# Performance work log

Measured on AMD Instinct MI355X. Metric: run time of the kernel, lower is better.

Reference implementation:

```python
import jax, jax.numpy as jnp
import numpy as np

B, N, D = 4, 4096, 256


def setup_inputs() -> dict:
    key = jax.random.key(0)
    ks = jax.random.split(key, 8)
    s = 0.05
    return {
        "x": jax.random.normal(ks[0], (B, N, D), dtype=jnp.float32),
        "z": jax.random.normal(ks[1], (B, N, D), dtype=jnp.float32),
        "Wq_w": jax.random.normal(ks[2], (D, D), dtype=jnp.float32) * s,
        "Wq_b": jax.random.normal(ks[3], (D,), dtype=jnp.float32) * s,
        "Wk_w": jax.random.normal(ks[4], (D, D), dtype=jnp.float32) * s,
        "Wk_b": jax.random.normal(ks[5], (D,), dtype=jnp.float32) * s,
        "Wv_w": jax.random.normal(ks[6], (D, D), dtype=jnp.float32) * s,
        "Wv_b": jax.random.normal(ks[7], (D,), dtype=jnp.float32) * s,
    }


def reference(x, z, Wq_w, Wq_b, Wk_w, Wk_b, Wv_w, Wv_b):
    # torch Linear: y = x @ W.T + b
    q = jnp.einsum("bnd,ed->bne", x, Wq_w) + Wq_b  # [B,N,D]
    k = jnp.einsum("bnd,ed->bne", z, Wk_w) + Wk_b  # [B,N,D]
    v = jnp.einsum("bnd,ed->bne", z, Wv_w) + Wv_b  # [B,N,D]
    inv_sqrt_d = 1.0 / jnp.sqrt(jnp.float32(q.shape[-1]))
    s = jnp.einsum("bqd,bkd->bqk", q, k) * inv_sqrt_d  # [B,N,N] scores
    attn = jax.nn.softmax(s, axis=-1)
    return jnp.einsum("bqk,bkd->bqd", attn, v)
```

## Files before the change

kernel.cpp:

```cpp
#include <hip/hip_runtime.h>
#include <hip/hip_bf16.h>
#include <math.h>

#define BATCH 4
#define SEQ   4096
#define DIM   256
#define AS1 __attribute__((address_space(1)))
#define AS3 __attribute__((address_space(3)))

typedef __attribute__((ext_vector_type(8))) short  bf16x8;
typedef __attribute__((ext_vector_type(4))) short  bf16x4;
typedef __attribute__((ext_vector_type(4))) float  f32x4;
typedef __attribute__((ext_vector_type(4))) int    i32x4;

#define LOG2E 1.44269504088896340736f
#define EXP2(x) __builtin_amdgcn_exp2f(x)

__device__ __forceinline__ short f2bf(float f) {
    union { float f; unsigned u; } v; v.f = f;
    unsigned r = (v.u + 0x7fffu + ((v.u >> 16) & 1u)) >> 16;
    return (short)r;
}

__device__ __forceinline__ int cvtpk(float lo, float hi) {
    int r;
    asm("v_cvt_pk_bf16_f32 %0, %1, %2" : "=v"(r) : "v"(lo), "v"(hi));
    return r;
}

__device__ __forceinline__ void gload_lds16(const void* g, void* l) {
    __builtin_amdgcn_global_load_lds((const AS1 void*)g, (AS3 void*)l, 16, 0, 0);
}

template<bool TRANS>
__global__ __launch_bounds__(512) void proj_kernel(
    const float* __restrict__ A,
    const float* __restrict__ W,
    const float* __restrict__ bias,
    unsigned short* __restrict__ out,
    float scale)
{
    __shared__ __align__(16) short Wlds[256 * 40];

    const int t    = threadIdx.x;
    const int wave = t >> 6, lane = t & 63;
    const int rw   = wave & 3, nh = wave >> 2;
    const int c    = lane & 15, g = lane >> 4;
    const int wrow = blockIdx.x * 64 + rw * 16;

    f32x4 acc[8];
    for (int nt = 0; nt < 8; ++nt) acc[nt] = f32x4{0.f, 0.f, 0.f, 0.f};

    f32x4 wpf[4];
    for (int i = 0; i < 4; ++i) {
        int f = i * 2048 + t * 4;
        wpf[i] = *(const f32x4*)&W[(f >> 5) * 256 + (f & 31)];
    }
    f32x4 a0 = *(const f32x4*)&A[(wrow + c) * 256 + g * 8];
    f32x4 a1 = *(const f32x4*)&A[(wrow + c) * 256 + g * 8 + 4];

    for (int ks = 0; ks < 8; ++ks) {
        __syncthreads();
        for (int i = 0; i < 4; ++i) {
            int f = i * 2048 + t * 4;
            bf16x4 s4;
            s4[0] = f2bf(wpf[i][0]); s4[1] = f2bf(wpf[i][1]);
            s4[2] = f2bf(wpf[i][2]); s4[3] = f2bf(wpf[i][3]);
            *(bf16x4*)&Wlds[(f >> 5) * 40 + (f & 31)] = s4;
        }
        __syncthreads();
        bf16x8 af;
        af[0] = f2bf(a0[0]); af[1] = f2bf(a0[1]); af[2] = f2bf(a0[2]); af[3] = f2bf(a0[3]);
        af[4] = f2bf(a1[0]); af[5] = f2bf(a1[1]); af[6] = f2bf(a1[2]); af[7] = f2bf(a1[3]);
        if (ks < 7) {
            for (int i = 0; i < 4; ++i) {
                int f = i * 2048 + t * 4;
                wpf[i] = *(const f32x4*)&W[(f >> 5) * 256 + (ks + 1) * 32 + (f & 31)];
            }
            a0 = *(const f32x4*)&A[(wrow + c) * 256 + (ks + 1) * 32 + g * 8];
            a1 = *(const f32x4*)&A[(wrow + c) * 256 + (ks + 1) * 32 + g * 8 + 4];
        }
        __builtin_amdgcn_s_setprio(1);
        for (int nt = 0; nt < 8; ++nt) {
            int e = (nh * 8 + nt) * 16 + c;
            bf16x8 bfr = *(const bf16x8*)&Wlds[e * 40 + g * 8];
            acc[nt] = __builtin_amdgcn_mfma_f32_16x16x32_bf16(af, bfr, acc[nt], 0, 0, 0);
        }
        __builtin_amdgcn_s_setprio(0);
    }

    if constexpr (TRANS) {
        const int nb = wrow >> 12, n0 = wrow & 4095;
        for (int nt = 0; nt < 8; ++nt) {
            int e = (nh * 8 + nt) * 16 + c;
            float bv = bias[e];
            bf16x4 s4;
            s4[0] = f2bf((acc[nt][0] + bv) * scale); s4[1] = f2bf((acc[nt][1] + bv) * scale);
            s4[2] = f2bf((acc[nt][2] + bv) * scale); s4[3] = f2bf((acc[nt][3] + bv) * scale);
            *(bf16x4*)&out[((size_t)nb * DIM + e) * SEQ + n0 + g * 4] = s4;
        }
    } else {
        for (int nt = 0; nt < 8; ++nt) {
            int e = (nh * 8 + nt) * 16 + c;
            float bv = bias[e];
            for (int j = 0; j < 4; ++j)
                out[(size_t)(wrow + g * 4 + j) * 256 + e] =
                    (unsigned short)f2bf((acc[nt][j] + bv) * scale);
        }
    }
}

__global__ __launch_bounds__(512) void kv_proj_kernel(
    const float* __restrict__ A,
    const float* __restrict__ Wk, const float* __restrict__ bk,
    const float* __restrict__ Wv, const float* __restrict__ bv,
    unsigned short* __restrict__ Kout,
    unsigned short* __restrict__ Vtout)
{
    __shared__ __align__(16) short WldsK[256 * 40];
    __shared__ __align__(16) short WldsV[256 * 40];

    const int t    = threadIdx.x;
    const int wave = t >> 6, lane = t & 63;
    const int rw   = wave & 3, nh = wave >> 2;
    const int c    = lane & 15, g = lane >> 4;
    const int wrow = blockIdx.x * 64 + rw * 16;

    f32x4 acck[8], accv[8];
    for (int nt = 0; nt < 8; ++nt) {
        acck[nt] = f32x4{0.f, 0.f, 0.f, 0.f};
        accv[nt] = f32x4{0.f, 0.f, 0.f, 0.f};
    }

    f32x4 wpfk[4], wpfv[4];
    for (int i = 0; i < 4; ++i) {
        int f = i * 2048 + t * 4;
        wpfk[i] = *(const f32x4*)&Wk[(f >> 5) * 256 + (f & 31)];
        wpfv[i] = *(const f32x4*)&Wv[(f >> 5) * 256 + (f & 31)];
    }
    f32x4 a0 = *(const f32x4*)&A[(wrow + c) * 256 + g * 8];
    f32x4 a1 = *(const f32x4*)&A[(wrow + c) * 256 + g * 8 + 4];

    for (int ks = 0; ks < 8; ++ks) {
        __syncthreads();
        for (int i = 0; i < 4; ++i) {
            int f = i * 2048 + t * 4;
            bf16x4 sk, sv;
            sk[0] = f2bf(wpfk[i][0]); sk[1] = f2bf(wpfk[i][1]);
            sk[2] = f2bf(wpfk[i][2]); sk[3] = f2bf(wpfk[i][3]);
            sv[0] = f2bf(wpfv[i][0]); sv[1] = f2bf(wpfv[i][1]);
            sv[2] = f2bf(wpfv[i][2]); sv[3] = f2bf(wpfv[i][3]);
            *(bf16x4*)&WldsK[(f >> 5) * 40 + (f & 31)] = sk;
            *(bf16x4*)&WldsV[(f >> 5) * 40 + (f & 31)] = sv;
        }
        __syncthreads();
        bf16x8 af;
        af[0] = f2bf(a0[0]); af[1] = f2bf(a0[1]); af[2] = f2bf(a0[2]); af[3] = f2bf(a0[3]);
        af[4] = f2bf(a1[0]); af[5] = f2bf(a1[1]); af[6] = f2bf(a1[2]); af[7] = f2bf(a1[3]);
        if (ks < 7) {
            for (int i = 0; i < 4; ++i) {
                int f = i * 2048 + t * 4;
                wpfk[i] = *(const f32x4*)&Wk[(f >> 5) * 256 + (ks + 1) * 32 + (f & 31)];
                wpfv[i] = *(const f32x4*)&Wv[(f >> 5) * 256 + (ks + 1) * 32 + (f & 31)];
            }
            a0 = *(const f32x4*)&A[(wrow + c) * 256 + (ks + 1) * 32 + g * 8];
            a1 = *(const f32x4*)&A[(wrow + c) * 256 + (ks + 1) * 32 + g * 8 + 4];
        }
        __builtin_amdgcn_s_setprio(1);
        for (int nt = 0; nt < 8; ++nt) {
            int e = (nh * 8 + nt) * 16 + c;
            bf16x8 bk_ = *(const bf16x8*)&WldsK[e * 40 + g * 8];
            acck[nt] = __builtin_amdgcn_mfma_f32_16x16x32_bf16(af, bk_, acck[nt], 0, 0, 0);
            bf16x8 bv_ = *(const bf16x8*)&WldsV[e * 40 + g * 8];
            accv[nt] = __builtin_amdgcn_mfma_f32_16x16x32_bf16(af, bv_, accv[nt], 0, 0, 0);
        }
        __builtin_amdgcn_s_setprio(0);
    }

    for (int nt = 0; nt < 8; ++nt) {
        int e = (nh * 8 + nt) * 16 + c;
        float bb = bk[e];
        for (int j = 0; j < 4; ++j)
            Kout[(size_t)(wrow + g * 4 + j) * 256 + e] =
                (unsigned short)f2bf(acck[nt][j] + bb);
    }
    const int nb = wrow >> 12, n0 = wrow & 4095;
    for (int nt = 0; nt < 8; ++nt) {
        int e = (nh * 8 + nt) * 16 + c;
        float bb = bv[e];
        bf16x4 s4;
        s4[0] = f2bf(accv[nt][0] + bb); s4[1] = f2bf(accv[nt][1] + bb);
        s4[2] = f2bf(accv[nt][2] + bb); s4[3] = f2bf(accv[nt][3] + bb);
        *(bf16x4*)&Vtout[((size_t)nb * DIM + e) * SEQ + n0 + g * 4] = s4;
    }
}

#define KVB 32

__global__ __launch_bounds__(256, 2) void fa2_kernel(
    const unsigned short* __restrict__ Q,
    const unsigned short* __restrict__ K,
    const unsigned short* __restrict__ Vt,
    unsigned short* __restrict__ Opart,
    float2* __restrict__ ml,
    int nsplit)
{
    __shared__ __align__(16) unsigned short Klds[2][KVB * 256];
    __shared__ __align__(16) unsigned short Vlds[2][256 * KVB];

    const int t = threadIdx.x;
    const int w = t >> 6, lane = t & 63;
    const int c = lane & 15, g = lane >> 4;

    int b, sidx, qt;
    if (nsplit == 4) {
        int xcd  = blockIdx.x & 7;
        int rest = blockIdx.x >> 3;
        int combo = (xcd << 1) | (rest >> 5);
        qt   = rest & 31;
        b    = combo >> 2;
        sidx = combo & 3;
    } else {
        qt   = blockIdx.x & 31;
        b    = blockIdx.x >> 5;
        sidx = 0;
    }
    const int ts = (sidx * 128) / nsplit;
    const int te = ((sidx + 1) * 128) / nsplit;

    const int wrow = qt * 128 + w * 32;

    bf16x8 qf[2][8];
    #pragma unroll
    for (int h = 0; h < 2; ++h) {
        const unsigned short* Qrow = &Q[((size_t)b * SEQ + wrow + 16 * h + c) * DIM];
        #pragma unroll
        for (int ks = 0; ks < 8; ++ks)
            qf[h][ks] = *(const bf16x8*)&Qrow[ks * 32 + g * 8];
    }

    f32x4 o[2][16];
    #pragma unroll
    for (int h = 0; h < 2; ++h)
        #pragma unroll
        for (int nt = 0; nt < 16; ++nt) o[h][nt] = f32x4{0.f, 0.f, 0.f, 0.f};
    float m[2]     = {-1e30f, -1e30f};
    float llane[2] = {0.f, 0.f};

    const char* Kb_ = (const char*)&K[(size_t)b * SEQ * DIM];
    const char* Vb_ = (const char*)&Vt[(size_t)b * DIM * SEQ];

    const int l31 = lane & 31;
    int koff[4], voff[4], dstb[4];
    const int vsw = ((lane >> 2) & 3) ^ ((lane >> 4) & 3);
    const int vcb = ((lane & 3) ^ vsw) << 4;
    #pragma unroll
    for (int ii = 0; ii < 4; ++ii) {
        int kr = 8 * w + 2 * ii + (lane >> 5);
        int sc = (kr & 3) | ((kr & 8) >> 1);
        koff[ii] = kr * 512 + ((l31 ^ sc) << 4);
        int vr = 64 * w + 16 * ii + (lane >> 2);
        voff[ii] = vr * (SEQ * 2) + vcb;
        dstb[ii] = (4 * w + ii) * 1024;
    }

    #define STAGE(kt_, buf_) do {                                              \
        const size_t kb_ = (size_t)(kt_) * (KVB * DIM * 2);                    \
        const size_t vb_ = (size_t)(kt_) * (KVB * 2);                          \
        _Pragma("unroll")                                                      \
        for (int ii = 0; ii < 4; ++ii) {                                       \
            gload_lds16(Kb_ + kb_ + koff[ii], (char*)&Klds[buf_][0] + dstb[ii]); \
            gload_lds16(Vb_ + vb_ + voff[ii], (char*)&Vlds[buf_][0] + dstb[ii]); \
        }                                                                      \
    } while (0)

    STAGE(ts, 0);
    int buf = 0;

    const int xk   = (c & 7) << 3;
    const int rphi = ((c & 3) + 8 * (c >> 2));
    const int vcol = (g * 8) ^ ((((c & 3) ^ ((c >> 2) & 3))) << 3);

    for (int kt = ts; kt < te; ++kt) {
        asm volatile("s_waitcnt vmcnt(0)" ::: "memory");
        __builtin_amdgcn_s_barrier();
        if (kt + 1 < te) STAGE(kt + 1, buf ^ 1);

        const unsigned short* Kl = &Klds[buf][0];
        const unsigned short* Vl = &Vlds[buf][0];

        f32x4 s[2][2];
        #pragma unroll
        for (int h = 0; h < 2; ++h) {
            s[h][0] = f32x4{0.f, 0.f, 0.f, 0.f};
            s[h][1] = f32x4{0.f, 0.f, 0.f, 0.f};
        }
        __builtin_amdgcn_s_setprio(1);
        #pragma unroll
        for (int ks = 0; ks < 8; ++ks) {
            int off = (ks * 32 + g * 8) ^ xk;
            bf16x8 kf0 = *(const bf16x8*)&Kl[rphi * 256 + off];
            bf16x8 kf1 = *(const bf16x8*)&Kl[(rphi + 4) * 256 + off];
            s[0][0] = __builtin_amdgcn_mfma_f32_16x16x32_bf16(kf0, qf[0][ks], s[0][0], 0, 0, 0);
            s[1][0] = __builtin_amdgcn_mfma_f32_16x16x32_bf16(kf0, qf[1][ks], s[1][0], 0, 0, 0);
            s[0][1] = __builtin_amdgcn_mfma_f32_16x16x32_bf16(kf1, qf[0][ks], s[0][1], 0, 0, 0);
            s[1][1] = __builtin_amdgcn_mfma_f32_16x16x32_bf16(kf1, qf[1][ks], s[1][1], 0, 0, 0);
        }
        __builtin_amdgcn_s_setprio(0);

        float pm[2];
        #pragma unroll
        for (int h = 0; h < 2; ++h)
            pm[h] = fmaxf(fmaxf(fmaxf(s[h][0][0], s[h][0][1]), fmaxf(s[h][0][2], s[h][0][3])),
                          fmaxf(fmaxf(s[h][1][0], s[h][1][1]), fmaxf(s[h][1][2], s[h][1][3])));
        bool ok = (pm[0] <= m[0] + 11.f) && (pm[1] <= m[1] + 11.f);
        if (!__all(ok)) {
            #pragma unroll
            for (int h = 0; h < 2; ++h) {
                float pr = pm[h];
                pr = fmaxf(pr, __shfl_xor(pr, 16));
                pr = fmaxf(pr, __shfl_xor(pr, 32));
                float mn = fmaxf(m[h], pr);
                float r  = EXP2(m[h] - mn);
                m[h] = mn; llane[h] *= r;
                float r0 = __shfl(r, g * 4 + 0), r1 = __shfl(r, g * 4 + 1);
                float r2 = __shfl(r, g * 4 + 2), r3 = __shfl(r, g * 4 + 3);
                #pragma unroll
                for (int nt = 0; nt < 16; ++nt) {
                    o[0][nt][0] *= (h == 0 ? r0 : 1.f);
                }
                if (h == 0) {
                    #pragma unroll
                    for (int nt = 0; nt < 16; ++nt) {
                        o[0][nt][0] *= r0; o[0][nt][1] *= r1;
                        o[0][nt][2] *= r2; o[0][nt][3] *= r3;
                    }
                } else {
                    #pragma unroll
                    for (int nt = 0; nt < 16; ++nt) {
                        o[1][nt][0] *= r0; o[1][nt][1] *= r1;
                        o[1][nt][2] *= r2; o[1][nt][3] *= r3;
                    }
                }
            }
        }
        bf16x8 pa0, pa1;
        {
            float p0 = EXP2(s[0][0][0] - m[0]), p1 = EXP2(s[0][0][1] - m[0]);
            float p2 = EXP2(s[0][0][2] - m[0]), p3 = EXP2(s[0][0][3] - m[0]);
            float p4 = EXP2(s[0][1][0] - m[0]), p5 = EXP2(s[0][1][1] - m[0]);
            float p6 = EXP2(s[0][1][2] - m[0]), p7 = EXP2(s[0][1][3] - m[0]);
            llane[0] += ((p0 + p1) + (p2 + p3)) + ((p4 + p5) + (p6 + p7));
            union { int d[4]; bf16x8 v; } u;
            u.d[0] = cvtpk(p0, p1); u.d[1] = cvtpk(p2, p3);
            u.d[2] = cvtpk(p4, p5); u.d[3] = cvtpk(p6, p7);
            pa0 = u.v;
        }
        {
            float p0 = EXP2(s[1][0][0] - m[1]), p1 = EXP2(s[1][0][1] - m[1]);
            float p2 = EXP2(s[1][0][2] - m[1]), p3 = EXP2(s[1][0][3] - m[1]);
            float p4 = EXP2(s[1][1][0] - m[1]), p5 = EXP2(s[1][1][1] - m[1]);
            float p6 = EXP2(s[1][1][2] - m[1]), p7 = EXP2(s[1][1][3] - m[1]);
            llane[1] += ((p0 + p1) + (p2 + p3)) + ((p4 + p5) + (p6 + p7));
            union { int d[4]; bf16x8 v; } u;
            u.d[0] = cvtpk(p0, p1); u.d[1] = cvtpk(p2, p3);
            u.d[2] = cvtpk(p4, p5); u.d[3] = cvtpk(p6, p7);
            pa1 = u.v;
        }

        __builtin_amdgcn_s_setprio(1);
        #pragma unroll
        for (int nt = 0; nt < 16; ++nt) {
            bf16x8 vf = *(const bf16x8*)&Vl[(nt * 16 + c) * 32 + vcol];
            o[0][nt] = __builtin_amdgcn_mfma_f32_16x16x32_bf16(pa0, vf, o[0][nt], 0, 0, 0);
            o[1][nt] = __builtin_amdgcn_mfma_f32_16x16x32_bf16(pa1, vf, o[1][nt], 0, 0, 0);
        }
        __builtin_amdgcn_s_setprio(0);
        buf ^= 1;
    }

    #pragma unroll
    for (int h = 0; h < 2; ++h) {
        float lsum = llane[h];
        lsum += __shfl_xor(lsum, 16);
        lsum += __shfl_xor(lsum, 32);
        float inv = 1.0f / lsum;
        float i0 = __shfl(inv, g * 4 + 0), i1 = __shfl(inv, g * 4 + 1);
        float i2 = __shfl(inv, g * 4 + 2), i3 = __shfl(inv, g * 4 + 3);

        const size_t obase = ((size_t)sidx * BATCH * SEQ + (size_t)b * SEQ + wrow + 16 * h) * DIM;
        for (int nt = 0; nt < 16; ++nt) {
            Opart[obase + (size_t)(g * 4 + 0) * DIM + nt * 16 + c] =
                (unsigned short)f2bf(o[h][nt][0] * i0);
            Opart[obase + (size_t)(g * 4 + 1) * DIM + nt * 16 + c] =
                (unsigned short)f2bf(o[h][nt][1] * i1);
            Opart[obase + (size_t)(g * 4 + 2) * DIM + nt * 16 + c] =
                (unsigned short)f2bf(o[h][nt][2] * i2);
            Opart[obase + (size_t)(g * 4 + 3) * DIM + nt * 16 + c] =
                (unsigned short)f2bf(o[h][nt][3] * i3);
        }
        if (g == 0) {
            ml[(size_t)sidx * BATCH * SEQ + (size_t)b * SEQ + wrow + 16 * h + c] =
                make_float2(m[h], lsum);
        }
    }
}

__global__ __launch_bounds__(256) void combine_kernel(
    const unsigned short* __restrict__ Opart, const float2* __restrict__ ml,
    float* __restrict__ out)
{
    const int t = threadIdx.x;
    const size_t row = (size_t)blockIdx.x * 4 + (t >> 6);
    const int lane = t & 63;

    float2 e[4];
    float M = -1e30f;
    for (int s = 0; s < 4; ++s) {
        e[s] = ml[(size_t)s * BATCH * SEQ + row];
        M = fmaxf(M, e[s].x);
    }
    float wgt[4], L = 0.f;
    for (int s = 0; s < 4; ++s) { wgt[s] = e[s].y * EXP2(e[s].x - M); L += wgt[s]; }
    float invL = 1.0f / L;

    f32x4 acc = f32x4{0.f, 0.f, 0.f, 0.f};
    for (int s = 0; s < 4; ++s) {
        bf16x4 v = *(const bf16x4*)&Opart[((size_t)s * BATCH * SEQ + row) * DIM + lane * 4];
        float ws = wgt[s] * invL;
        union { unsigned u; float f; } c0, c1, c2, c3;
        c0.u = ((unsigned)(unsigned short)v[0]) << 16;
        c1.u = ((unsigned)(unsigned short)v[1]) << 16;
        c2.u = ((unsigned)(unsigned short)v[2]) << 16;
        c3.u = ((unsigned)(unsigned short)v[3]) << 16;
        acc[0] += ws * c0.f; acc[1] += ws * c1.f;
        acc[2] += ws * c2.f; acc[3] += ws * c3.f;
    }
    *(f32x4*)&out[row * DIM + lane * 4] = acc;
}

__global__ void expand_kernel(const unsigned short* __restrict__ in,
                              float* __restrict__ o) {
    size_t i = (size_t)blockIdx.x * blockDim.x + threadIdx.x;
    union { unsigned u; float f; } v;
    v.u = ((unsigned)in[i]) << 16;
    o[i] = v.f;
}

extern "C" void kernel_launch(void* const* d_in, const int* in_sizes, int n_in,
                              void* d_out, int out_size, void* d_ws, size_t ws_size,
                              hipStream_t stream) {
    const float* x  = (const float*)d_in[0];
    const float* z  = (const float*)d_in[1];
    const float* Wq = (const float*)d_in[2];
    const float* bq = (const float*)d_in[3];
    const float* Wk = (const float*)d_in[4];
    const float* bk = (const float*)d_in[5];
    const float* Wv = (const float*)d_in[6];
    const float* bv = (const float*)d_in[7];
    float* out = (float*)d_out;

    const size_t TENS = (size_t)BATCH * SEQ * DIM;
    unsigned short* Qb  = (unsigned short*)d_ws;
    unsigned short* Kb  = Qb + TENS;
    unsigned short* Vtb = Kb + TENS;

    const size_t base_bytes = 3 * TENS * sizeof(unsigned short);
    const size_t need4 = base_bytes + 4 * TENS * sizeof(unsigned short)
                       + 4 * (size_t)BATCH * SEQ * sizeof(float2);
    const int nsplit = (ws_size >= need4) ? 4 : 1;

    const float qscale = 0.0625f * LOG2E;

    proj_kernel<false><<<256, 512, 0, stream>>>(x, Wq, bq, Qb, qscale);
    kv_proj_kernel<<<256, 512, 0, stream>>>(z, Wk, bk, Wv, bv, Kb, Vtb);

    if (nsplit == 4) {
        unsigned short* Op = (unsigned short*)((char*)d_ws + base_bytes);
        float2* mlb = (float2*)((char*)d_ws + base_bytes + 4 * TENS * sizeof(unsigned short));
        fa2_kernel<<<512, 256, 0, stream>>>(Qb, Kb, Vtb, Op, mlb, 4);
        combine_kernel<<<4096, 256, 0, stream>>>(Op, mlb, out);
    } else {
        unsigned short* Op = (unsigned short*)((char*)d_ws + base_bytes);
        float2* mlb = (float2*)((char*)d_ws + base_bytes + TENS * sizeof(unsigned short));
        fa2_kernel<<<128, 256, 0, stream>>>(Qb, Kb, Vtb, Op, mlb, 1);
        expand_kernel<<<TENS / 256, 256, 0, stream>>>(Op, out);
    }
}
```

Before: 122.9 us.

## Merge Q and KV projections into one launch, widen combine loads

Folds the Q projection and the fused K/V projection into a single 512-block launch, with the first 256 blocks computing Q and the rest computing K and V. This removes one kernel launch and lets both projections share the GPU at once. It also deletes a redundant per-tile rescale loop in the attention kernel that multiplied o[0] by r0, a multiply the following h==0 block appears to perform as well. The combine kernel now has each lane handle 8 bf16 values with 16-byte loads and launches half as many blocks. The merged kernel always allocates LDS for two weight tiles, which may reduce occupancy for the Q blocks.

```diff
diff --git a/kernel.cpp b/kernel.cpp
--- a/kernel.cpp
+++ b/kernel.cpp
@@ -32,166 +32,146 @@
     __builtin_amdgcn_global_load_lds((const AS1 void*)g, (AS3 void*)l, 16, 0, 0);
 }
 
-template<bool TRANS>
-__global__ __launch_bounds__(512) void proj_kernel(
-    const float* __restrict__ A,
-    const float* __restrict__ W,
-    const float* __restrict__ bias,
-    unsigned short* __restrict__ out,
-    float scale)
+__global__ __launch_bounds__(512) void qkv_proj_kernel(
+    const float* __restrict__ x, const float* __restrict__ z,
+    const float* __restrict__ Wq, const float* __restrict__ bq,
+    const float* __restrict__ Wk, const float* __restrict__ bk,
+    const float* __restrict__ Wv, const float* __restrict__ bv,
+    unsigned short* __restrict__ Qout,
+    unsigned short* __restrict__ Kout,
+    unsigned short* __restrict__ Vtout,
+    float qscale)
 {
-    __shared__ __align__(16) short Wlds[256 * 40];
+    __shared__ __align__(16) short WldsA[256 * 40];
+    __shared__ __align__(16) short WldsB[256 * 40];
 
     const int t    = threadIdx.x;
     const int wave = t >> 6, lane = t & 63;
     const int rw   = wave & 3, nh = wave >> 2;
     const int c    = lane & 15, g = lane >> 4;
-    const int wrow = blockIdx.x * 64 + rw * 16;
-
-    f32x4 acc[8];
-    for (int nt = 0; nt < 8; ++nt) acc[nt] = f32x4{0.f, 0.f, 0.f, 0.f};
-
-    f32x4 wpf[4];
-    for (int i = 0; i < 4; ++i) {
-        int f = i * 2048 + t * 4;
-        wpf[i] = *(const f32x4*)&W[(f >> 5) * 256 + (f & 31)];
-    }
-    f32x4 a0 = *(const f32x4*)&A[(wrow + c) * 256 + g * 8];
-    f32x4 a1 = *(const f32x4*)&A[(wrow + c) * 256 + g * 8 + 4];
-
-    for (int ks = 0; ks < 8; ++ks) {
-        __syncthreads();
+
+    if (blockIdx.x < 256) {
+        const int wrow = blockIdx.x * 64 + rw * 16;
+        f32x4 acc[8];
+        #pragma unroll
+        for (int nt = 0; nt < 8; ++nt) acc[nt] = f32x4{0.f, 0.f, 0.f, 0.f};
+
+        f32x4 wpf[4];
         for (int i = 0; i < 4; ++i) {
             int f = i * 2048 + t * 4;
-            bf16x4 s4;
-            s4[0] = f2bf(wpf[i][0]); s4[1] = f2bf(wpf[i][1]);
-            s4[2] = f2bf(wpf[i][2]); s4[3] = f2bf(wpf[i][3]);
-            *(bf16x4*)&Wlds[(f >> 5) * 40 + (f & 31)] = s4;
-        }
-        __syncthreads();
-        bf16x8 af;
-        af[0] = f2bf(a0[0]); af[1] = f2bf(a0[1]); af[2] = f2bf(a0[2]); af[3] = f2bf(a0[3]);
-        af[4] = f2bf(a1[0]); af[5] = f2bf(a1[1]); af[6] = f2bf(a1[2]); af[7] = f2bf(a1[3]);
-        if (ks < 7) {
+            wpf[i] = *(const f32x4*)&Wq[(f >> 5) * 256 + (f & 31)];
+        }
+        f32x4 a0 = *(const f32x4*)&x[(wrow + c) * 256 + g * 8];
+        f32x4 a1 = *(const f32x4*)&x[(wrow + c) * 256 + g * 8 + 4];
+
+        for (int ks = 0; ks < 8; ++ks) {
+            __syncthreads();
             for (int i = 0; i < 4; ++i) {
                 int f = i * 2048 + t * 4;
-                wpf[i] = *(const f32x4*)&W[(f >> 5) * 256 + (ks + 1) * 32 + (f & 31)];
-            }
-            a0 = *(const f32x4*)&A[(wrow + c) * 256 + (ks + 1) * 32 + g * 8];
-            a1 = *(const f32x4*)&A[(wrow + c) * 256 + (ks + 1) * 32 + g * 8 + 4];
-        }
-        __builtin_amdgcn_s_setprio(1);
+                bf16x4 s4;
+                s4[0] = f2bf(wpf[i][0]); s4[1] = f2bf(wpf[i][1]);
+                s4[2] = f2bf(wpf[i][2]); s4[3] = f2bf(wpf[i][3]);
+                *(bf16x4*)&WldsA[(f >> 5) * 40 + (f & 31)] = s4;
+            }
+            __syncthreads();
+            bf16x8 af;
+            af[0] = f2bf(a0[0]); af[1] = f2bf(a0[1]); af[2] = f2bf(a0[2]); af[3] = f2bf(a0[3]);
+            af[4] = f2bf(a1[0]); af[5] = f2bf(a1[1]); af[6] = f2bf(a1[2]); af[7] = f2bf(a1[3]);
+            if (ks < 7) {
+                for (int i = 0; i < 4; ++i) {
+                    int f = i * 2048 + t * 4;
+                    wpf[i] = *(const f32x4*)&Wq[(f >> 5) * 256 + (ks + 1) * 32 + (f & 31)];
+                }
+                a0 = *(const f32x4*)&x[(wrow + c) * 256 + (ks + 1) * 32 + g * 8];
+                a1 = *(const f32x4*)&x[(wrow + c) * 256 + (ks + 1) * 32 + g * 8 + 4];
+            }
+            __builtin_amdgcn_s_setprio(1);
+            #pragma unroll
+            for (int nt = 0; nt < 8; ++nt) {
+                int e = (nh * 8 + nt) * 16 + c;
+                bf16x8 bfr = *(const bf16x8*)&WldsA[e * 40 + g * 8];
+                acc[nt] = __builtin_amdgcn_mfma_f32_16x16x32_bf16(af, bfr, acc[nt], 0, 0, 0);
+            }
+            __builtin_amdgcn_s_setprio(0);
+        }
         for (int nt = 0; nt < 8; ++nt) {
             int e = (nh * 8 + nt) * 16 + c;
-            bf16x8 bfr = *(const bf16x8*)&Wlds[e * 40 + g * 8];
-            acc[nt] = __builtin_amdgcn_mfma_f32_16x16x32_bf16(af, bfr, acc[nt], 0, 0, 0);
-        }
-        __builtin_amdgcn_s_setprio(0);
-    }
-
-    if constexpr (TRANS) {
+            float bv_ = bq[e];
+            for (int j = 0; j < 4; ++j)
+                Qout[(size_t)(wrow + g * 4 + j) * 256 + e] =
+                    (unsigned short)f2bf((acc[nt][j] + bv_) * qscale);
+        }
+    } else {
+        const int wrow = (blockIdx.x - 256) * 64 + rw * 16;
+        f32x4 acck[8], accv[8];
+        #pragma unroll
+        for (int nt = 0; nt < 8; ++nt) {
+            acck[nt] = f32x4{0.f, 0.f, 0.f, 0.f};
+            accv[nt] = f32x4{0.f, 0.f, 0.f, 0.f};
+        }
+
+        f32x4 wpfk[4], wpfv[4];
+        for (int i = 0; i < 4; ++i) {
+            int f = i * 2048 + t * 4;
+            wpfk[i] = *(const f32x4*)&Wk[(f >> 5) * 256 + (f & 31)];
+            wpfv[i] = *(const f32x4*)&Wv[(f >> 5) * 256 + (f & 31)];
+        }
+        f32x4 a0 = *(const f32x4*)&z[(wrow + c) * 256 + g * 8];
+        f32x4 a1 = *(const f32x4*)&z[(wrow + c) * 256 + g * 8 + 4];
+
+        for (int ks = 0; ks < 8; ++ks) {
+            __syncthreads();
+            for (int i = 0; i < 4; ++i) {
+                int f = i * 2048 + t * 4;
+                bf16x4 sk, sv;
+                sk[0] = f2bf(wpfk[i][0]); sk[1] = f2bf(wpfk[i][1]);
+                sk[2] = f2bf(wpfk[i][2]); sk[3] = f2bf(wpfk[i][3]);
+                sv[0] = f2bf(wpfv[i][0]); sv[1] = f2bf(wpfv[i][1]);
+                sv[2] = f2bf(wpfv[i][2]); sv[3] = f2bf(wpfv[i][3]);
+                *(bf16x4*)&WldsA[(f >> 5) * 40 + (f & 31)] = sk;
+                *(bf16x4*)&WldsB[(f >> 5) * 40 + (f & 31)] = sv;
+            }
+            __syncthreads();
+            bf16x8 af;
+            af[0] = f2bf(a0[0]); af[1] = f2bf(a0[1]); af[2] = f2bf(a0[2]); af[3] = f2bf(a0[3]);
+            af[4] = f2bf(a1[0]); af[5] = f2bf(a1[1]); af[6] = f2bf(a1[2]); af[7] = f2bf(a1[3]);
+            if (ks < 7) {
+                for (int i = 0; i < 4; ++i) {
+                    int f = i * 2048 + t * 4;
+                    wpfk[i] = *(const f32x4*)&Wk[(f >> 5) * 256 + (ks + 1) * 32 + (f & 31)];
+                    wpfv[i] = *(const f32x4*)&Wv[(f >> 5) * 256 + (ks + 1) * 32 + (f & 31)];
+                }
+                a0 = *(const f32x4*)&z[(wrow + c) * 256 + (ks + 1) * 32 + g * 8];
+                a1 = *(const f32x4*)&z[(wrow + c) * 256 + (ks + 1) * 32 + g * 8 + 4];
+            }
+            __builtin_amdgcn_s_setprio(1);
+            #pragma unroll
+            for (int nt = 0; nt < 8; ++nt) {
+                int e = (nh * 8 + nt) * 16 + c;
+                bf16x8 bk_ = *(const bf16x8*)&WldsA[e * 40 + g * 8];
+                acck[nt] = __builtin_amdgcn_mfma_f32_16x16x32_bf16(af, bk_, acck[nt], 0, 0, 0);
+                bf16x8 bv_ = *(const bf16x8*)&WldsB[e * 40 + g * 8];
+                accv[nt] = __builtin_amdgcn_mfma_f32_16x16x32_bf16(af, bv_, accv[nt], 0, 0, 0);
+            }
+            __builtin_amdgcn_s_setprio(0);
+        }
+
+        for (int nt = 0; nt < 8; ++nt) {
+            int e = (nh * 8 + nt) * 16 + c;
+            float bb = bk[e];
+            for (int j = 0; j < 4; ++j)
+                Kout[(size_t)(wrow + g * 4 + j) * 256 + e] =
+                    (unsigned short)f2bf(acck[nt][j] + bb);
+        }
         const int nb = wrow >> 12, n0 = wrow & 4095;
         for (int nt = 0; nt < 8; ++nt) {
             int e = (nh * 8 + nt) * 16 + c;
-            float bv = bias[e];
+            float bb = bv[e];
             bf16x4 s4;
-            s4[0] = f2bf((acc[nt][0] + bv) * scale); s4[1] = f2bf((acc[nt][1] + bv) * scale);
-            s4[2] = f2bf((acc[nt][2] + bv) * scale); s4[3] = f2bf((acc[nt][3] + bv) * scale);
-            *(bf16x4*)&out[((size_t)nb * DIM + e) * SEQ + n0 + g * 4] = s4;
-        }
-    } else {
-        for (int nt = 0; nt < 8; ++nt) {
-            int e = (nh * 8 + nt) * 16 + c;
-            float bv = bias[e];
-            for (int j = 0; j < 4; ++j)
-                out[(size_t)(wrow + g * 4 + j) * 256 + e] =
-                    (unsigned short)f2bf((acc[nt][j] + bv) * scale);
-        }
-    }
-}
-
-__global__ __launch_bounds__(512) void kv_proj_kernel(
-    const float* __restrict__ A,
-    const float* __restrict__ Wk, const float* __restrict__ bk,
-    const float* __restrict__ Wv, const float* __restrict__ bv,
-    unsigned short* __restrict__ Kout,
-    unsigned short* __restrict__ Vtout)
-{
-    __shared__ __align__(16) short WldsK[256 * 40];
-    __shared__ __align__(16) short WldsV[256 * 40];
-
-    const int t    = threadIdx.x;
-    const int wave = t >> 6, lane = t & 63;
-    const int rw   = wave & 3, nh = wave >> 2;
-    const int c    = lane & 15, g = lane >> 4;
-    const int wrow = blockIdx.x * 64 + rw * 16;
-
-    f32x4 acck[8], accv[8];
-    for (int nt = 0; nt < 8; ++nt) {
-        acck[nt] = f32x4{0.f, 0.f, 0.f, 0.f};
-        accv[nt] = f32x4{0.f, 0.f, 0.f, 0.f};
-    }
-
-    f32x4 wpfk[4], wpfv[4];
-    for (int i = 0; i < 4; ++i) {
-        int f = i * 2048 + t * 4;
-        wpfk[i] = *(const f32x4*)&Wk[(f >> 5) * 256 + (f & 31)];
-        wpfv[i] = *(const f32x4*)&Wv[(f >> 5) * 256 + (f & 31)];
-    }
-    f32x4 a0 = *(const f32x4*)&A[(wrow + c) * 256 + g * 8];
-    f32x4 a1 = *(const f32x4*)&A[(wrow + c) * 256 + g * 8 + 4];
-
-    for (int ks = 0; ks < 8; ++ks) {
-        __syncthreads();
-        for (int i = 0; i < 4; ++i) {
-            int f = i * 2048 + t * 4;
-            bf16x4 sk, sv;
-            sk[0] = f2bf(wpfk[i][0]); sk[1] = f2bf(wpfk[i][1]);
-            sk[2] = f2bf(wpfk[i][2]); sk[3] = f2bf(wpfk[i][3]);
-            sv[0] = f2bf(wpfv[i][0]); sv[1] = f2bf(wpfv[i][1]);
-            sv[2] = f2bf(wpfv[i][2]); sv[3] = f2bf(wpfv[i][3]);
-            *(bf16x4*)&WldsK[(f >> 5) * 40 + (f & 31)] = sk;
-            *(bf16x4*)&WldsV[(f >> 5) * 40 + (f & 31)] = sv;
-        }
-        __syncthreads();
-        bf16x8 af;
-        af[0] = f2bf(a0[0]); af[1] = f2bf(a0[1]); af[2] = f2bf(a0[2]); af[3] = f2bf(a0[3]);
-        af[4] = f2bf(a1[0]); af[5] = f2bf(a1[1]); af[6] = f2bf(a1[2]); af[7] = f2bf(a1[3]);
-        if (ks < 7) {
-            for (int i = 0; i < 4; ++i) {
-                int f = i * 2048 + t * 4;
-                wpfk[i] = *(const f32x4*)&Wk[(f >> 5) * 256 + (ks + 1) * 32 + (f & 31)];
-                wpfv[i] = *(const f32x4*)&Wv[(f >> 5) * 256 + (ks + 1) * 32 + (f & 31)];
-            }
-            a0 = *(const f32x4*)&A[(wrow + c) * 256 + (ks + 1) * 32 + g * 8];
-            a1 = *(const f32x4*)&A[(wrow + c) * 256 + (ks + 1) * 32 + g * 8 + 4];
-        }
-        __builtin_amdgcn_s_setprio(1);
-        for (int nt = 0; nt < 8; ++nt) {
-            int e = (nh * 8 + nt) * 16 + c;
-            bf16x8 bk_ = *(const bf16x8*)&WldsK[e * 40 + g * 8];
-            acck[nt] = __builtin_amdgcn_mfma_f32_16x16x32_bf16(af, bk_, acck[nt], 0, 0, 0);
-            bf16x8 bv_ = *(const bf16x8*)&WldsV[e * 40 + g * 8];
-            accv[nt] = __builtin_amdgcn_mfma_f32_16x16x32_bf16(af, bv_, accv[nt], 0, 0, 0);
-        }
-        __builtin_amdgcn_s_setprio(0);
-    }
-
-    for (int nt = 0; nt < 8; ++nt) {
-        int e = (nh * 8 + nt) * 16 + c;
-        float bb = bk[e];
-        for (int j = 0; j < 4; ++j)
-            Kout[(size_t)(wrow + g * 4 + j) * 256 + e] =
-                (unsigned short)f2bf(acck[nt][j] + bb);
-    }
-    const int nb = wrow >> 12, n0 = wrow & 4095;
-    for (int nt = 0; nt < 8; ++nt) {
-        int e = (nh * 8 + nt) * 16 + c;
-        float bb = bv[e];
-        bf16x4 s4;
-        s4[0] = f2bf(accv[nt][0] + bb); s4[1] = f2bf(accv[nt][1] + bb);
-        s4[2] = f2bf(accv[nt][2] + bb); s4[3] = f2bf(accv[nt][3] + bb);
-        *(bf16x4*)&Vtout[((size_t)nb * DIM + e) * SEQ + n0 + g * 4] = s4;
+            s4[0] = f2bf(accv[nt][0] + bb); s4[1] = f2bf(accv[nt][1] + bb);
+            s4[2] = f2bf(accv[nt][2] + bb); s4[3] = f2bf(accv[nt][3] + bb);
+            *(bf16x4*)&Vtout[((size_t)nb * DIM + e) * SEQ + n0 + g * 4] = s4;
+        }
     }
 }
 
@@ -325,10 +305,6 @@
                 m[h] = mn; llane[h] *= r;
                 float r0 = __shfl(r, g * 4 + 0), r1 = __shfl(r, g * 4 + 1);
                 float r2 = __shfl(r, g * 4 + 2), r3 = __shfl(r, g * 4 + 3);
-                #pragma unroll
-                for (int nt = 0; nt < 16; ++nt) {
-                    o[0][nt][0] *= (h == 0 ? r0 : 1.f);
-                }
                 if (h == 0) {
                     #pragma unroll
                     for (int nt = 0; nt < 16; ++nt) {
@@ -411,32 +387,38 @@
     float* __restrict__ out)
 {
     const int t = threadIdx.x;
-    const size_t row = (size_t)blockIdx.x * 4 + (t >> 6);
-    const int lane = t & 63;
+    const size_t row = (size_t)blockIdx.x * 8 + (t >> 5);
+    const int lane = t & 31;
 
     float2 e[4];
     float M = -1e30f;
+    #pragma unroll
     for (int s = 0; s < 4; ++s) {
         e[s] = ml[(size_t)s * BATCH * SEQ + row];
         M = fmaxf(M, e[s].x);
     }
     float wgt[4], L = 0.f;
+    #pragma unroll
     for (int s = 0; s < 4; ++s) { wgt[s] = e[s].y * EXP2(e[s].x - M); L += wgt[s]; }
     float invL = 1.0f / L;
 
-    f32x4 acc = f32x4{0.f, 0.f, 0.f, 0.f};
+    float acc[8] = {0.f, 0.f, 0.f, 0.f, 0.f, 0.f, 0.f, 0.f};
+    #pragma unroll
     for (int s = 0; s < 4; ++s) {
-        bf16x4 v = *(const bf16x4*)&Opart[((size_t)s * BATCH * SEQ + row) * DIM + lane * 4];
+        bf16x8 v = *(const bf16x8*)&Opart[((size_t)s * BATCH * SEQ + row) * DIM + lane * 8];
         float ws = wgt[s] * invL;
-        union { unsigned u; float f; } c0, c1, c2, c3;
-        c0.u = ((unsigned)(unsigned short)v[0]) << 16;
-        c1.u = ((unsigned)(unsigned short)v[1]) << 16;
-        c2.u = ((unsigned)(unsigned short)v[2]) << 16;
-        c3.u = ((unsigned)(unsigned short)v[3]) << 16;
-        acc[0] += ws * c0.f; acc[1] += ws * c1.f;
-        acc[2] += ws * c2.f; acc[3] += ws * c3.f;
-    }
-    *(f32x4*)&out[row * DIM + lane * 4] = acc;
+        #pragma unroll
+        for (int j = 0; j < 8; ++j) {
+            union { unsigned u; float f; } cv;
+            cv.u = ((unsigned)(unsigned short)v[j]) << 16;
+            acc[j] += ws * cv.f;
+        }
+    }
+    f32x4 o0, o1;
+    o0[0] = acc[0]; o0[1] = acc[1]; o0[2] = acc[2]; o0[3] = acc[3];
+    o1[0] = acc[4]; o1[1] = acc[5]; o1[2] = acc[6]; o1[3] = acc[7];
+    *(f32x4*)&out[row * DIM + lane * 8]     = o0;
+    *(f32x4*)&out[row * DIM + lane * 8 + 4] = o1;
 }
 
 __global__ void expand_kernel(const unsigned short* __restrict__ in,
@@ -472,14 +454,14 @@
 
     const float qscale = 0.0625f * LOG2E;
 
-    proj_kernel<false><<<256, 512, 0, stream>>>(x, Wq, bq, Qb, qscale);
-    kv_proj_kernel<<<256, 512, 0, stream>>>(z, Wk, bk, Wv, bv, Kb, Vtb);
+    qkv_proj_kernel<<<512, 512, 0, stream>>>(x, z, Wq, bq, Wk, bk, Wv, bv,
+                                             Qb, Kb, Vtb, qscale);
 
     if (nsplit == 4) {
         unsigned short* Op = (unsigned short*)((char*)d_ws + base_bytes);
         float2* mlb = (float2*)((char*)d_ws + base_bytes + 4 * TENS * sizeof(unsigned short));
         fa2_kernel<<<512, 256, 0, stream>>>(Qb, Kb, Vtb, Op, mlb, 4);
-        combine_kernel<<<4096, 256, 0, stream>>>(Op, mlb, out);
+        combine_kernel<<<2048, 256, 0, stream>>>(Op, mlb, out);
     } else {
         unsigned short* Op = (unsigned short*)((char*)d_ws + base_bytes);
         float2* mlb = (float2*)((char*)d_ws + base_bytes + TENS * sizeof(unsigned short));
```

Measured after the change: 118.9 us. 3.2% less time.
